# Optimization experiments

Hardware: AMD Instinct MI355X
Metric: run time of the kernel (lower is better)

The kernel has to match this reference:

```python
import jax, jax.numpy as jnp
import numpy as np

B = 8; C = 128; EXP = 4; H = 112; W = 112; K = 3; PAD = 1; STRIDE = 1
IN_C = C * EXP  # 512
EPS = 1e-5


def setup_inputs() -> dict:
    key = jax.random.key(0)
    ks = jax.random.split(key, 24)
    f32 = jnp.float32

    def n(k, shape, s=0.05):
        return jax.random.normal(k, shape, f32) * s

    def bn_params(k):
        k1, k2, k3, k4 = jax.random.split(k, 4)
        g = 1.0 + 0.1 * jax.random.normal(k1, (), f32)  # placeholder, per-channel below
        return k1, k2, k3, k4

    inp = {}
    inp["x"] = jax.random.normal(ks[0], (B, IN_C, H, W), f32)
    # conv1: 1x1, 512 -> 128
    inp["w1"] = n(ks[1], (C, IN_C))
    inp["b1"] = n(ks[2], (C,))
    # bn1
    inp["g1"] = 1.0 + 0.1 * jax.random.normal(ks[3], (C,), f32)
    inp["be1"] = 0.1 * jax.random.normal(ks[4], (C,), f32)
    inp["m1"] = 0.1 * jax.random.normal(ks[5], (C,), f32)
    inp["v1"] = 1.0 + 0.1 * jax.random.uniform(ks[6], (C,), f32)
    # offset conv: 3x3, C -> 18 (small weights so sampling offsets stay modest)
    inp["woff"] = n(ks[7], (2 * K * K, C, K, K), 0.01)
    inp["boff"] = jnp.zeros((2 * K * K,), f32)
    # deformable conv weight: 3x3, C -> C
    inp["wd"] = n(ks[8], (C, C, K, K))
    inp["bd"] = n(ks[9], (C,))
    # bn2
    inp["g2"] = 1.0 + 0.1 * jax.random.normal(ks[10], (C,), f32)
    inp["be2"] = 0.1 * jax.random.normal(ks[11], (C,), f32)
    inp["m2"] = 0.1 * jax.random.normal(ks[12], (C,), f32)
    inp["v2"] = 1.0 + 0.1 * jax.random.uniform(ks[13], (C,), f32)
    # conv2: 1x1, 128 -> 512
    inp["w2"] = n(ks[14], (IN_C, C))
    inp["b2"] = n(ks[15], (IN_C,))
    # bn3
    inp["g3"] = 1.0 + 0.1 * jax.random.normal(ks[16], (IN_C,), f32)
    inp["be3"] = 0.1 * jax.random.normal(ks[17], (IN_C,), f32)
    inp["m3"] = 0.1 * jax.random.normal(ks[18], (IN_C,), f32)
    inp["v3"] = 1.0 + 0.1 * jax.random.uniform(ks[19], (IN_C,), f32)
    return inp


def conv1x1(x, w, b):
    return jnp.einsum("oc,bchw->bohw", w, x) + b[None, :, None, None]


def bn(x, g, be, m, v):
    inv = g / jnp.sqrt(v + EPS)
    return x * inv[None, :, None, None] + (be - m * inv)[None, :, None, None]


def conv3x3(x, w, b):
    out = jax.lax.conv_general_dilated(
        x, w, (STRIDE, STRIDE), ((PAD, PAD), (PAD, PAD)),
        dimension_numbers=("NCHW", "OIHW", "NCHW"))
    return out + b[None, :, None, None]


def deform_conv(x, offset, w, b):
    # x: [B, Cin, H, W]; offset: [B, 2*K*K, Ho, Wo] (y,x interleaved per kernel pt)
    Bn, Cin, Hh, Ww = x.shape
    Ho, Wo = offset.shape[2], offset.shape[3]
    P = Ho * Wo
    off = offset.reshape(Bn, K * K, 2, Ho, Wo)
    kk = jnp.arange(K * K)
    ky = (kk // K).astype(jnp.float32)  # 0..2
    kx = (kk % K).astype(jnp.float32)
    base_y = jnp.arange(Ho, dtype=jnp.float32) * STRIDE - PAD
    base_x = jnp.arange(Wo, dtype=jnp.float32) * STRIDE - PAD
    py = base_y[None, None, :, None] + ky[None, :, None, None] + off[:, :, 0]  # [B,9,Ho,Wo]
    px = base_x[None, None, None, :] + kx[None, :, None, None] + off[:, :, 1]
    y0 = jnp.floor(py); x0 = jnp.floor(px)
    dy = (py - y0).reshape(Bn, 1, -1)  # [B,1,9*P]
    dx = (px - x0).reshape(Bn, 1, -1)
    x_flat = x.reshape(Bn, Cin, Hh * Ww)

    def gather(yi, xi):
        valid = ((yi >= 0) & (yi <= Hh - 1) & (xi >= 0) & (xi <= Ww - 1))
        yc = jnp.clip(yi, 0, Hh - 1).astype(jnp.int32)
        xc = jnp.clip(xi, 0, Ww - 1).astype(jnp.int32)
        idx = (yc * Ww + xc).reshape(Bn, -1)  # [B, 9*P]
        g = jax.vmap(lambda xb, ib: xb[:, ib])(x_flat, idx)  # [B, Cin, 9*P]
        return g * valid.reshape(Bn, 1, -1).astype(x.dtype)

    v00 = gather(y0, x0)
    v01 = gather(y0, x0 + 1)
    v10 = gather(y0 + 1, x0)
    v11 = gather(y0 + 1, x0 + 1)
    cols = (v00 * (1 - dy) * (1 - dx) + v01 * (1 - dy) * dx
            + v10 * dy * (1 - dx) + v11 * dy * dx)  # [B, Cin, 9*P]
    cols = cols.reshape(Bn, Cin * K * K, P)
    out = jnp.einsum("oi,bip->bop", w.reshape(w.shape[0], -1), cols)
    out = out + b[None, :, None]
    return out.reshape(Bn, w.shape[0], Ho, Wo)


def reference(x, w1, b1, g1, be1, m1, v1, woff, boff, wd, bd,
              g2, be2, m2, v2, w2, b2, g3, be3, m3, v3):
    out = jax.nn.relu(bn(conv1x1(x, w1, b1), g1, be1, m1, v1))
    offset = conv3x3(out, woff, boff)
    out = deform_conv(out, offset, wd, bd)
    out = bn(out, g2, be2, m2, v2)
    out = bn(conv1x1(out, w2, b2), g3, be3, m3, v3)
    return jax.nn.relu(out + x)
```

## Files before the change

kernel.cpp:

```cpp
#include <hip/hip_runtime.h>
#include <hip/hip_bf16.h>


typedef __attribute__((ext_vector_type(8))) short short8;
typedef __attribute__((ext_vector_type(4))) float f32x4;

constexpr int Bn = 8;
constexpr int IC = 512;
constexpr int Cc = 128;
constexpr int Hh = 112;
constexpr int Ww = 112;
constexpr int Pp = Hh * Ww;
constexpr float EPSf = 1e-5f;

constexpr size_t OFS_OUT2B = 2097152;
constexpr size_t OFS_W1B   = (size_t)Bn * Pp * IC / 2;
constexpr size_t OFS_W2B   = OFS_W1B + (size_t)Cc * IC / 2;
constexpr size_t OFS_WDB   = OFS_W2B + (size_t)IC * Cc / 2;
constexpr size_t OFS_WOFB  = OFS_WDB + (size_t)9 * Cc * Cc / 2;

__device__ __forceinline__ ushort f2bf(float f) {
  uint u = __float_as_uint(f);
  return (ushort)((u + 0x7fffu + ((u >> 16) & 1u)) >> 16);
}
__device__ __forceinline__ float bfLO(uint u) {
  return __uint_as_float(u << 16);
}
__device__ __forceinline__ float bfHI(uint u) {
  return __uint_as_float(u & 0xffff0000u);
}
__device__ __forceinline__ uint cvtpk(float a, float b) {
  __hip_bfloat162 h = __float22bfloat162_rn(make_float2(a, b));
  return *(uint*)&h;
}

__global__ __launch_bounds__(256) void prep_kernel(
    const float* __restrict__ w1, const float* __restrict__ w2,
    const float* __restrict__ wd, const float* __restrict__ woff,
    float* __restrict__ ws) {
  ushort* w1b  = (ushort*)(ws + OFS_W1B);
  ushort* w2b  = (ushort*)(ws + OFS_W2B);
  ushort* wdb  = (ushort*)(ws + OFS_WDB);
  ushort* wofb = (ushort*)(ws + OFS_WOFB);
  const int n1 = Cc * IC;
  const int n2 = IC * Cc;
  const int n3 = 9 * Cc * Cc;
  const int n4 = 9 * 32 * Cc;
  const int total = n1 + n2 + n3 + n4;
  for (int idx = blockIdx.x * blockDim.x + threadIdx.x; idx < total;
       idx += gridDim.x * blockDim.x) {
    if (idx < n1) {
      w1b[idx] = f2bf(w1[idx]);
    } else if (idx < n1 + n2) {
      int t = idx - n1;
      w2b[t] = f2bf(w2[t]);
    } else if (idx < n1 + n2 + n3) {
      int t = idx - n1 - n2;
      int k = t / (Cc * Cc), r = t % (Cc * Cc);
      int oc = r / Cc, ic = r % Cc;
      wdb[t] = f2bf(wd[(oc * Cc + ic) * 9 + k]);
    } else {
      int t = idx - n1 - n2 - n3;
      int k = t / (32 * Cc), r = t % (32 * Cc);
      int oc = r / Cc, ic = r % Cc;
      wofb[t] = (oc < 18) ? f2bf(woff[(oc * Cc + ic) * 9 + k]) : (ushort)0;
    }
  }
}

__global__ __launch_bounds__(256) void k1_fused_mfma(
    const float* __restrict__ x, const ushort* __restrict__ w1b,
    const float* __restrict__ b1, const float* __restrict__ g1,
    const float* __restrict__ be1, const float* __restrict__ m1,
    const float* __restrict__ v1, ushort* __restrict__ out1b) {
  __shared__ ushort smem[26624];

  const int tid = threadIdx.x;
  const int lane = tid & 63;
  const int wv = tid >> 6;
  const int lr = lane & 15, lg = lane >> 4;
  const int orig = blockIdx.x;
  const int bid = (orig & 7) * 98 + (orig >> 3);
  const int bi = bid / 98;
  const int pblk = (bid % 98) * 128;

  float xs[2][4][2][2];
  short8 wsv[2][2];

#define BAR_LGKM asm volatile("s_waitcnt lgkmcnt(0)\ns_barrier" ::: "memory")

#define LOADX(c, s)                                                       \
  {                                                                       \
    const float* xb_ = x + ((size_t)bi * IC + (size_t)((c) * 32 + wv * 8)) * Pp \
                         + pblk + lane;                                   \
    _Pragma("unroll") for (int q = 0; q < 4; ++q) {                       \
      _Pragma("unroll") for (int p = 0; p < 2; ++p) {                     \
        xs[s][q][p][0] = xb_[(size_t)(2 * q + p) * Pp];                   \
        xs[s][q][p][1] = xb_[(size_t)(2 * q + p) * Pp + 64];              \
      }                                                                   \
    }                                                                     \
  }

#define LOADW(c, s)                                                       \
  {                                                                       \
    const ushort* wb_ = w1b + (size_t)(wv * 32 + (lane >> 2)) * IC        \
                            + (c) * 32 + (lane & 3) * 8;                  \
    wsv[s][0] = *(const short8*)(wb_);                                    \
    wsv[s][1] = *(const short8*)(wb_ + (size_t)16 * IC);                  \
  }

#define WRITE(c, s)                                                       \
  {                                                                       \
    char* atb_ = (char*)smem + ((c) & 1) * 16384;                         \
    _Pragma("unroll") for (int e = 0; e < 2; ++e) {                       \
      const int px_ = lane + 64 * e;                                      \
      uint4 pk_;                                                          \
      uint* pp_ = (uint*)&pk_;                                            \
      _Pragma("unroll") for (int q = 0; q < 4; ++q)                       \
        pp_[q] = cvtpk(xs[s][q][0][e], xs[s][q][1][e]);                   \
      *(uint4*)(atb_ + px_ * 128 + ((wv ^ (px_ & 7)) << 4)) = pk_;        \
    }                                                                     \
    ushort* wlb_ = smem + 16384 + ((c) & 1) * 5120;                       \
    *(short8*)(wlb_ + (wv * 32 + (lane >> 2)) * 40 + (lane & 3) * 8) = wsv[s][0]; \
    *(short8*)(wlb_ + (wv * 32 + 16 + (lane >> 2)) * 40 + (lane & 3) * 8) = wsv[s][1]; \
  }

  f32x4 acc[2][8];
#pragma unroll
  for (int m = 0; m < 2; ++m)
#pragma unroll
    for (int n = 0; n < 8; ++n) acc[m][n] = (f32x4)0.f;

  LOADX(0, 0) LOADW(0, 0)
  LOADX(1, 1) LOADW(1, 1)

#pragma unroll
  for (int c = 0; c < 16; ++c) {
    WRITE(c, c & 1);
    BAR_LGKM;
    if (c + 2 < 16) { LOADX(c + 2, c & 1) LOADW(c + 2, c & 1) }

    {
      const char* atb = (const char*)smem + (c & 1) * 16384;
      const ushort* wlb = smem + 16384 + (c & 1) * 5120;
      const int sw = (lg ^ (lr & 7)) << 4;
      short8 a0 = *(const short8*)(atb + (wv * 32 + lr) * 128 + sw);
      short8 a1 = *(const short8*)(atb + (wv * 32 + 16 + lr) * 128 + sw);
#pragma unroll
      for (int n = 0; n < 8; ++n) {
        short8 b = *(const short8*)(wlb + (n * 16 + lr) * 40 + lg * 8);
        acc[0][n] = __builtin_amdgcn_mfma_f32_16x16x32_bf16(a0, b, acc[0][n], 0, 0, 0);
        acc[1][n] = __builtin_amdgcn_mfma_f32_16x16x32_bf16(a1, b, acc[1][n], 0, 0, 0);
      }
    }
  }

#undef LOADX
#undef LOADW
#undef WRITE
#undef BAR_LGKM

  __syncthreads();

  ushort(*Ab)[136] = (ushort(*)[136])smem;
#pragma unroll
  for (int n = 0; n < 8; ++n) {
    int oc = n * 16 + lr;
    float inv = g1[oc] * rsqrtf(v1[oc] + EPSf);
    float sh = (b1[oc] - m1[oc]) * inv + be1[oc];
#pragma unroll
    for (int m = 0; m < 2; ++m) {
#pragma unroll
      for (int r = 0; r < 4; ++r) {
        int pl = wv * 32 + m * 16 + lg * 4 + r;
        Ab[pl][oc] = f2bf(fmaxf(acc[m][n][r] * inv + sh, 0.f));
      }
    }
  }
#pragma unroll
  for (int j = 0; j < 8; ++j) {
    int pl = wv * 32 + j * 4 + (lane >> 4);
    uint4 v = *(const uint4*)&Ab[pl][(lane & 15) * 8];
    *(uint4*)(out1b + ((size_t)bi * Pp + pblk + pl) * Cc + (lane & 15) * 8) = v;
  }
}

__global__ __launch_bounds__(256) void k3_deform_mfma(
    const ushort* __restrict__ out1b, const ushort* __restrict__ wofb,
    const float* __restrict__ boff,
    const ushort* __restrict__ wdb, const float* __restrict__ bd,
    const float* __restrict__ g2, const float* __restrict__ be2,
    const float* __restrict__ m2, const float* __restrict__ v2,
    ushort* __restrict__ out2b) {
  __shared__ ushort colsA[2][64][136];
  __shared__ float meta[9 * 64 * 8];

  const int tid = threadIdx.x;
  const int lane = tid & 63;
  const int wv = tid >> 6;
  const int lr = lane & 15, lg = lane >> 4;
  const int orig = blockIdx.x;
  const int bid = (orig & 7) * 196 + (orig >> 3);
  const int bi = bid / 196;
  const int p0 = (bid % 196) * 64;

  const ushort* src = out1b + (size_t)bi * Pp * Cc;
  float* pacc = (float*)colsA;

  {
    int ohm[4], owm[4];
#pragma unroll
    for (int m = 0; m < 4; ++m) {
      int p = p0 + m * 16 + lr;
      ohm[m] = p / Ww;
      owm[m] = p - ohm[m] * Ww;
    }
    f32x4 aco[4][2];
#pragma unroll
    for (int m = 0; m < 4; ++m) { aco[m][0] = (f32x4)0.f; aco[m][1] = (f32x4)0.f; }

    for (int k = wv; k < 9; k += 4) {
      const int kdy = k / 3 - 1, kdx = k % 3 - 1;
      const ushort* rp[4];
      bool val[4];
#pragma unroll
      for (int m = 0; m < 4; ++m) {
        int yy = ohm[m] + kdy, xx = owm[m] + kdx;
        val[m] = ((unsigned)yy < (unsigned)Hh) && ((unsigned)xx < (unsigned)Ww);
        int yc = min(max(yy, 0), Hh - 1), xc = min(max(xx, 0), Ww - 1);
        rp[m] = src + (size_t)(yc * Ww + xc) * Cc;
      }
#pragma unroll
      for (int ks = 0; ks < 4; ++ks) {
        short8 b0 = *(const short8*)(wofb + (size_t)(k * 32 + lr) * Cc + ks * 32 + 8 * lg);
        short8 b1v = *(const short8*)(wofb + (size_t)(k * 32 + 16 + lr) * Cc + ks * 32 + 8 * lg);
#pragma unroll
        for (int m = 0; m < 4; ++m) {
          short8 av = *(const short8*)(rp[m] + ks * 32 + 8 * lg);
          short8 a = val[m] ? av : (short8)0;
          aco[m][0] = __builtin_amdgcn_mfma_f32_16x16x32_bf16(a, b0, aco[m][0], 0, 0, 0);
          aco[m][1] = __builtin_amdgcn_mfma_f32_16x16x32_bf16(a, b1v, aco[m][1], 0, 0, 0);
        }
      }
    }
#pragma unroll
    for (int n = 0; n < 2; ++n)
#pragma unroll
      for (int m = 0; m < 4; ++m)
#pragma unroll
        for (int r = 0; r < 4; ++r) {
          int px = m * 16 + lg * 4 + r;
          pacc[(wv * 64 + px) * 33 + n * 16 + lr] = aco[m][n][r];
        }
  }
  __syncthreads();

  {
    const int p = p0 + lane;
    const int oh = p / Ww, ow = p - oh * Ww;
    for (int k = wv; k < 9; k += 4) {
      const int kdy = k / 3 - 1, kdx = k % 3 - 1;
      float offy = boff[2 * k], offx = boff[2 * k + 1];
#pragma unroll
      for (int w = 0; w < 4; ++w) {
        offy += pacc[(w * 64 + lane) * 33 + 2 * k];
        offx += pacc[(w * 64 + lane) * 33 + 2 * k + 1];
      }
      float py = (float)(oh + kdy) + offy;
      float pxf = (float)(ow + kdx) + offx;
      float y0f = floorf(py), x0f = floorf(pxf);
      float dy = py - y0f, dx = pxf - x0f;
      int y0 = (int)y0f, x0 = (int)x0f;
      int y1 = y0 + 1, x1 = x0 + 1;
      float wy0 = (y0 >= 0 && y0 < Hh) ? 1.f - dy : 0.f;
      float wy1 = (y1 >= 0 && y1 < Hh) ? dy : 0.f;
      float wx0 = (x0 >= 0 && x0 < Ww) ? 1.f - dx : 0.f;
      float wx1 = (x1 >= 0 && x1 < Ww) ? dx : 0.f;
      int yc0 = min(max(y0, 0), Hh - 1), yc1 = min(max(y1, 0), Hh - 1);
      int xc0 = min(max(x0, 0), Ww - 1), xc1 = min(max(x1, 0), Ww - 1);
      float* mp = &meta[(k * 64 + lane) * 8];
      mp[0] = wy0 * wx0;
      mp[1] = wy0 * wx1;
      mp[2] = wy1 * wx0;
      mp[3] = wy1 * wx1;
      int* ip = (int*)(mp + 4);
      ip[0] = (yc0 * Ww + xc0) * (Cc * 2);
      ip[1] = (yc0 * Ww + xc1) * (Cc * 2);
      ip[2] = (yc1 * Ww + xc0) * (Cc * 2);
      ip[3] = (yc1 * Ww + xc1) * (Cc * 2);
    }
  }
  __syncthreads();

  f32x4 acc[4][2];
#pragma unroll
  for (int m = 0; m < 4; ++m) { acc[m][0] = (f32x4)0.f; acc[m][1] = (f32x4)0.f; }

  const int pxq = lane >> 4;
  const int l16 = lane & 15;
  const char* sb = (const char*)src + l16 * 16;

  uint4 gv[4][4];
  float4 gw[4];

#define BAR_LGKM asm volatile("s_waitcnt lgkmcnt(0)\ns_barrier" ::: "memory")

#define ISSUE(kk, t)                                                     \
  {                                                                      \
    const int px_ = wv * 16 + (t) * 4 + pxq;                             \
    const float* mp_ = &meta[((kk) * 64 + px_) * 8];                     \
    gw[t] = *(const float4*)mp_;                                         \
    int4 o4_ = *(const int4*)(mp_ + 4);                                  \
    gv[t][0] = *(const uint4*)(sb + o4_.x);                              \
    gv[t][1] = *(const uint4*)(sb + o4_.y);                              \
    gv[t][2] = *(const uint4*)(sb + o4_.z);                              \
    gv[t][3] = *(const uint4*)(sb + o4_.w);                              \
  }

#define COMMIT(buf, t)                                                   \
  {                                                                      \
    const int px_ = wv * 16 + (t) * 4 + pxq;                             \
    float4 w4_ = gw[t];                                                  \
    uint4 pk_;                                                           \
    uint* pkp_ = (uint*)&pk_;                                            \
    _Pragma("unroll")                                                    \
    for (int j = 0; j < 4; ++j) {                                        \
      uint a0_ = ((const uint*)&gv[t][0])[j];                            \
      uint a1_ = ((const uint*)&gv[t][1])[j];                            \
      uint a2_ = ((const uint*)&gv[t][2])[j];                            \
      uint a3_ = ((const uint*)&gv[t][3])[j];                            \
      float lo_ = w4_.x * bfLO(a0_) + w4_.y * bfLO(a1_)                  \
                + w4_.z * bfLO(a2_) + w4_.w * bfLO(a3_);                 \
      float hi_ = w4_.x * bfHI(a0_) + w4_.y * bfHI(a1_)                  \
                + w4_.z * bfHI(a2_) + w4_.w * bfHI(a3_);                 \
      pkp_[j] = cvtpk(lo_, hi_);                                         \
    }                                                                    \
    *(uint4*)&colsA[buf][px_][l16 * 8] = pk_;                            \
  }

  ISSUE(0, 0) ISSUE(0, 1) ISSUE(0, 2) ISSUE(0, 3)
  COMMIT(0, 0) COMMIT(0, 1) COMMIT(0, 2) COMMIT(0, 3)
  ISSUE(1, 0) ISSUE(1, 1) ISSUE(1, 2) ISSUE(1, 3)
  BAR_LGKM;

  for (int k = 0; k < 9; ++k) {
    const int cur = k & 1;
    const int nxt = cur ^ 1;
    const ushort* wk = wdb + (size_t)k * Cc * Cc + (size_t)(wv * 32) * Cc;

#pragma unroll
    for (int ks = 0; ks < 4; ++ks) {
      short8 b0 = *(const short8*)(wk + lr * Cc + ks * 32 + 8 * lg);
      short8 b1v = *(const short8*)(wk + (16 + lr) * Cc + ks * 32 + 8 * lg);
#pragma unroll
      for (int m = 0; m < 4; ++m) {
        short8 a = *(const short8*)&colsA[cur][m * 16 + lr][ks * 32 + 8 * lg];
        acc[m][0] = __builtin_amdgcn_mfma_f32_16x16x32_bf16(a, b0, acc[m][0], 0, 0, 0);
        acc[m][1] = __builtin_amdgcn_mfma_f32_16x16x32_bf16(a, b1v, acc[m][1], 0, 0, 0);
      }
    }

    if (k < 8) {
      COMMIT(nxt, 0)
      if (k < 7) { ISSUE(k + 2, 0) }
      COMMIT(nxt, 1)
      if (k < 7) { ISSUE(k + 2, 1) }
      COMMIT(nxt, 2)
      if (k < 7) { ISSUE(k + 2, 2) }
      COMMIT(nxt, 3)
      if (k < 7) { ISSUE(k + 2, 3) }
      BAR_LGKM;
    }
  }

#undef ISSUE
#undef COMMIT
#undef BAR_LGKM

#pragma unroll
  for (int n = 0; n < 2; ++n) {
    int oc = wv * 32 + n * 16 + lr;
    float inv = g2[oc] * rsqrtf(v2[oc] + EPSf);
    float sh = (bd[oc] - m2[oc]) * inv + be2[oc];
#pragma unroll
    for (int m = 0; m < 4; ++m) {
#pragma unroll
      for (int r = 0; r < 4; ++r) {
        int p = p0 + m * 16 + lg * 4 + r;
        out2b[((size_t)bi * Pp + p) * Cc + oc] = f2bf(acc[m][n][r] * inv + sh);
      }
    }
  }
}

__global__ __launch_bounds__(256, 2) void k4_mfma(
    const ushort* __restrict__ out2b, const ushort* __restrict__ w2b,
    const float* __restrict__ b2, const float* __restrict__ g3,
    const float* __restrict__ be3, const float* __restrict__ m3,
    const float* __restrict__ v3, const float* __restrict__ x,
    float* __restrict__ out) {
  __shared__ float obuf[2][16][260];

  const int tid = threadIdx.x;
  const int lane = tid & 63;
  const int wv = tid >> 6;
  const int lr = lane & 15, lg = lane >> 4;
  const int orig = blockIdx.x;
  const int bid = (orig & 7) * 392 + (orig >> 3);
  const int bi = bid / 392;
  const int r392 = bid % 392;
  const int oc_t = r392 / 49;
  const int pblk = (r392 % 49) * 256;
  const int p0 = pblk + wv * 64;
  const int ocb = oc_t * 64;

  const ushort* A = out2b + ((size_t)bi * Pp + p0) * Cc;
  const ushort* Bw = w2b + (size_t)ocb * Cc;

  f32x4 acc[4][4];
#pragma unroll
  for (int m = 0; m < 4; ++m)
#pragma unroll
    for (int n = 0; n < 4; ++n) acc[m][n] = (f32x4)0.f;

#pragma unroll
  for (int ks = 0; ks < 4; ++ks) {
    short8 a[4];
#pragma unroll
    for (int m = 0; m < 4; ++m)
      a[m] = *(const short8*)(A + (size_t)(m * 16 + lr) * Cc + ks * 32 + 8 * lg);
#pragma unroll
    for (int n = 0; n < 4; ++n) {
      short8 b = *(const short8*)(Bw + (size_t)(n * 16 + lr) * Cc + ks * 32 + 8 * lg);
#pragma unroll
      for (int m = 0; m < 4; ++m)
        acc[m][n] = __builtin_amdgcn_mfma_f32_16x16x32_bf16(a[m], b, acc[m][n], 0, 0, 0);
    }
  }

  float4 xv[2][4];

#define BARL asm volatile("s_waitcnt lgkmcnt(0)\ns_barrier" ::: "memory")
#define LOADXV(n, s)                                                      \
  {                                                                       \
    _Pragma("unroll") for (int it = 0; it < 4; ++it) {                    \
      int oc_ = ocb + (n) * 16 + it * 4 + wv;                             \
      xv[s][it] = *(const float4*)(x + ((size_t)bi * IC + oc_) * Pp       \
                                   + pblk + lane * 4);                    \
    }                                                                     \
  }

  LOADXV(0, 0)

#pragma unroll
  for (int n = 0; n < 4; ++n) {
    {
      int ocw = ocb + n * 16 + lr;
      float inv = g3[ocw] * rsqrtf(v3[ocw] + EPSf);
      float sh = (b2[ocw] - m3[ocw]) * inv + be3[ocw];
      float(*buf)[260] = obuf[n & 1];
#pragma unroll
      for (int m = 0; m < 4; ++m) {
        float4 o;
        o.x = acc[m][n][0] * inv + sh;
        o.y = acc[m][n][1] * inv + sh;
        o.z = acc[m][n][2] * inv + sh;
        o.w = acc[m][n][3] * inv + sh;
        *(float4*)&buf[lr][wv * 64 + m * 16 + lg * 4] = o;
      }
    }
    if (n < 3) { LOADXV(n + 1, (n + 1) & 1) }
    BARL;
    {
      const float(*buf)[260] = obuf[n & 1];
#pragma unroll
      for (int it = 0; it < 4; ++it) {
        int r = it * 4 + wv;
        int oc = ocb + n * 16 + r;
        float4 v = *(const float4*)&buf[r][lane * 4];
        float4 xr = xv[n & 1][it];
        float4 o;
        o.x = fmaxf(v.x + xr.x, 0.f);
        o.y = fmaxf(v.y + xr.y, 0.f);
        o.z = fmaxf(v.z + xr.z, 0.f);
        o.w = fmaxf(v.w + xr.w, 0.f);
        *(float4*)(out + ((size_t)bi * IC + oc) * Pp + pblk + lane * 4) = o;
      }
    }
  }
#undef BARL
#undef LOADXV
}

extern "C" void kernel_launch(void* const* d_in, const int* in_sizes, int n_in,
                              void* d_out, int out_size, void* d_ws, size_t ws_size,
                              hipStream_t stream) {
  const float* x    = (const float*)d_in[0];
  const float* w1   = (const float*)d_in[1];
  const float* b1   = (const float*)d_in[2];
  const float* g1   = (const float*)d_in[3];
  const float* be1  = (const float*)d_in[4];
  const float* m1   = (const float*)d_in[5];
  const float* v1   = (const float*)d_in[6];
  const float* woff = (const float*)d_in[7];
  const float* boff = (const float*)d_in[8];
  const float* wd   = (const float*)d_in[9];
  const float* bd   = (const float*)d_in[10];
  const float* g2   = (const float*)d_in[11];
  const float* be2  = (const float*)d_in[12];
  const float* m2   = (const float*)d_in[13];
  const float* v2   = (const float*)d_in[14];
  const float* w2   = (const float*)d_in[15];
  const float* b2   = (const float*)d_in[16];
  const float* g3   = (const float*)d_in[17];
  const float* be3  = (const float*)d_in[18];
  const float* m3   = (const float*)d_in[19];
  const float* v3   = (const float*)d_in[20];

  float* ws   = (float*)d_ws;
  float* out  = (float*)d_out;
  ushort* out2b = (ushort*)(ws + OFS_OUT2B);
  ushort* w1b   = (ushort*)(ws + OFS_W1B);
  ushort* w2b   = (ushort*)(ws + OFS_W2B);
  ushort* wdb   = (ushort*)(ws + OFS_WDB);
  ushort* wofb  = (ushort*)(ws + OFS_WOFB);
  ushort* out1b = (ushort*)d_out;

  prep_kernel<<<512, 256, 0, stream>>>(w1, w2, wd, woff, ws);
  k1_fused_mfma<<<Bn * 98, 256, 0, stream>>>(x, w1b, b1, g1, be1, m1, v1, out1b);
  k3_deform_mfma<<<Bn * 196, 256, 0, stream>>>(out1b, wofb, boff, wdb, bd,
                                               g2, be2, m2, v2, out2b);
  k4_mfma<<<Bn * 392, 256, 0, stream>>>(out2b, w2b, b2, g3, be3, m3, v3, x, out);
}
```

Measured before the change: 310.8 us.

## Split deform conv GEMM by pixel rows per wave to drop barriers

The deformable-conv MFMA loop now gives each wave its own 16 pixels and all 128 output channels, instead of all 64 pixels and a 32-channel slice. Each wave fills and reads only its own private column buffer in shared memory, so the per-tap block barriers are removed. The cost is that every wave now loads the full weight slice for each tap, which is four times more global/L2 weight traffic per block. The MFMA count per wave is unchanged.

```diff
diff --git a/kernel.cpp b/kernel.cpp
--- a/kernel.cpp
+++ b/kernel.cpp
@@ -192,7 +192,7 @@
     const float* __restrict__ g2, const float* __restrict__ be2,
     const float* __restrict__ m2, const float* __restrict__ v2,
     ushort* __restrict__ out2b) {
-  __shared__ ushort colsA[2][64][136];
+  __shared__ ushort colsA[4][2][16][136];
   __shared__ float meta[9 * 64 * 8];
 
   const int tid = threadIdx.x;
@@ -292,9 +292,9 @@
   }
   __syncthreads();
 
-  f32x4 acc[4][2];
-#pragma unroll
-  for (int m = 0; m < 4; ++m) { acc[m][0] = (f32x4)0.f; acc[m][1] = (f32x4)0.f; }
+  f32x4 acc[8];
+#pragma unroll
+  for (int n = 0; n < 8; ++n) acc[n] = (f32x4)0.f;
 
   const int pxq = lane >> 4;
   const int l16 = lane & 15;
@@ -302,8 +302,6 @@
 
   uint4 gv[4][4];
   float4 gw[4];
-
-#define BAR_LGKM asm volatile("s_waitcnt lgkmcnt(0)\ns_barrier" ::: "memory")
 
 #define ISSUE(kk, t)                                                     \
   {                                                                      \
@@ -319,7 +317,6 @@
 
 #define COMMIT(buf, t)                                                   \
   {                                                                      \
-    const int px_ = wv * 16 + (t) * 4 + pxq;                             \
     float4 w4_ = gw[t];                                                  \
     uint4 pk_;                                                           \
     uint* pkp_ = (uint*)&pk_;                                            \
@@ -335,28 +332,25 @@
                 + w4_.z * bfHI(a2_) + w4_.w * bfHI(a3_);                 \
       pkp_[j] = cvtpk(lo_, hi_);                                         \
     }                                                                    \
-    *(uint4*)&colsA[buf][px_][l16 * 8] = pk_;                            \
+    *(uint4*)&colsA[wv][buf][(t) * 4 + pxq][l16 * 8] = pk_;              \
   }
 
   ISSUE(0, 0) ISSUE(0, 1) ISSUE(0, 2) ISSUE(0, 3)
   COMMIT(0, 0) COMMIT(0, 1) COMMIT(0, 2) COMMIT(0, 3)
   ISSUE(1, 0) ISSUE(1, 1) ISSUE(1, 2) ISSUE(1, 3)
-  BAR_LGKM;
 
   for (int k = 0; k < 9; ++k) {
     const int cur = k & 1;
     const int nxt = cur ^ 1;
-    const ushort* wk = wdb + (size_t)k * Cc * Cc + (size_t)(wv * 32) * Cc;
+    const ushort* wk = wdb + (size_t)k * Cc * Cc;
 
 #pragma unroll
     for (int ks = 0; ks < 4; ++ks) {
-      short8 b0 = *(const short8*)(wk + lr * Cc + ks * 32 + 8 * lg);
-      short8 b1v = *(const short8*)(wk + (16 + lr) * Cc + ks * 32 + 8 * lg);
-#pragma unroll
-      for (int m = 0; m < 4; ++m) {
-        short8 a = *(const short8*)&colsA[cur][m * 16 + lr][ks * 32 + 8 * lg];
-        acc[m][0] = __builtin_amdgcn_mfma_f32_16x16x32_bf16(a, b0, acc[m][0], 0, 0, 0);
-        acc[m][1] = __builtin_amdgcn_mfma_f32_16x16x32_bf16(a, b1v, acc[m][1], 0, 0, 0);
+      short8 a = *(const short8*)&colsA[wv][cur][lr][ks * 32 + 8 * lg];
+#pragma unroll
+      for (int n = 0; n < 8; ++n) {
+        short8 b = *(const short8*)(wk + (size_t)(n * 16 + lr) * Cc + ks * 32 + 8 * lg);
+        acc[n] = __builtin_amdgcn_mfma_f32_16x16x32_bf16(a, b, acc[n], 0, 0, 0);
       }
     }
 
@@ -369,26 +363,21 @@
       if (k < 7) { ISSUE(k + 2, 2) }
       COMMIT(nxt, 3)
       if (k < 7) { ISSUE(k + 2, 3) }
-      BAR_LGKM;
     }
   }
 
 #undef ISSUE
 #undef COMMIT
-#undef BAR_LGKM
-
-#pragma unroll
-  for (int n = 0; n < 2; ++n) {
-    int oc = wv * 32 + n * 16 + lr;
+
+#pragma unroll
+  for (int n = 0; n < 8; ++n) {
+    int oc = n * 16 + lr;
     float inv = g2[oc] * rsqrtf(v2[oc] + EPSf);
     float sh = (bd[oc] - m2[oc]) * inv + be2[oc];
 #pragma unroll
-    for (int m = 0; m < 4; ++m) {
-#pragma unroll
-      for (int r = 0; r < 4; ++r) {
-        int p = p0 + m * 16 + lg * 4 + r;
-        out2b[((size_t)bi * Pp + p) * Cc + oc] = f2bf(acc[m][n][r] * inv + sh);
-      }
+    for (int r = 0; r < 4; ++r) {
+      int p = p0 + wv * 16 + lg * 4 + r;
+      out2b[((size_t)bi * Pp + p) * Cc + oc] = f2bf(acc[n][r] * inv + sh);
     }
   }
 }
```

Result: slower. 473.2 us (+52.3%).
